# Performance work log

Measured on AMD Instinct MI355X. Metric: run time of the kernel, lower is better.

The kernel has to match this reference:

```python
import jax, jax.numpy as jnp
import numpy as np

LAMBDA_SINK = 0.05  # temperature
NUM_SINK = 10       # Sinkhorn iterations


def setup_inputs() -> dict:
    key = jax.random.key(0)
    log_alpha = jax.random.normal(key, (8, 2048, 2048), dtype=jnp.float32)
    return {"log_alpha": log_alpha}


def reference(log_alpha):
    # gumbel_sinkhorn(log_alpha, temp=lambda_sink, n_iter=num_sink, slack=False)
    la = log_alpha / LAMBDA_SINK

    def body(la, _):
        # row normalization: subtract logsumexp over columns (dim=2)
        la = la - jax.nn.logsumexp(la, axis=2, keepdims=True)
        # column normalization: subtract logsumexp over rows (dim=1)
        la = la - jax.nn.logsumexp(la, axis=1, keepdims=True)
        return la, None

    la, _ = jax.lax.scan(body, la, None, length=NUM_SINK)
    return jnp.exp(la)  # doubly-stochastic (approx) matrix
```

## Files before the change

### kernel.cpp

```cpp
#include <hip/hip_runtime.h>
#include <math.h>

#define NB 8
#define NN 2048
#define SCALE2 28.853900817779268f
#define RPW 8
#define BROWS 32
#define CHB (NN / BROWS)

#if __has_builtin(__builtin_amdgcn_exp2f)
__device__ __forceinline__ float fexp2(float x) { return __builtin_amdgcn_exp2f(x); }
#else
__device__ __forceinline__ float fexp2(float x) { return exp2f(x); }
#endif
#if __has_builtin(__builtin_amdgcn_logf)
__device__ __forceinline__ float flog2(float x) { return __builtin_amdgcn_logf(x); }
#else
__device__ __forceinline__ float flog2(float x) { return log2f(x); }
#endif

__device__ __forceinline__ float wave_max(float x) {
#pragma unroll
    for (int off = 32; off >= 1; off >>= 1)
        x = fmaxf(x, __shfl_xor(x, off, 64));
    return x;
}
__device__ __forceinline__ float wave_sum(float x) {
#pragma unroll
    for (int off = 32; off >= 1; off >>= 1)
        x += __shfl_xor(x, off, 64);
    return x;
}

__global__ __launch_bounds__(256, 2) void fused_iter(const float* __restrict__ A,
                                                     const float* __restrict__ v,
                                                     float* __restrict__ u,
                                                     float* __restrict__ ps) {
    const int wid  = threadIdx.x >> 6;
    const int lane = threadIdx.x & 63;
    const int b    = blockIdx.x >> 6;
    const int blk  = blockIdx.x & 63;
    const int row0 = blk * BROWS + wid * RPW;

    float vv[32];
    {
        const float4* v4 = (const float4*)(v + (size_t)b * NN);
#pragma unroll
        for (int k = 0; k < 8; ++k) {
            float4 t = v4[lane + (k << 6)];
            vv[4 * k + 0] = t.x; vv[4 * k + 1] = t.y;
            vv[4 * k + 2] = t.z; vv[4 * k + 3] = t.w;
        }
    }

    float s[32];
#pragma unroll
    for (int i = 0; i < 32; ++i) s[i] = 0.f;

    float nxt[32];
    {
        const float4* a4 = (const float4*)(A + ((size_t)b * NN + row0) * NN);
#pragma unroll
        for (int k = 0; k < 8; ++k) {
            float4 a = a4[lane + (k << 6)];
            nxt[4 * k + 0] = a.x; nxt[4 * k + 1] = a.y;
            nxt[4 * k + 2] = a.z; nxt[4 * k + 3] = a.w;
        }
    }

#pragma unroll 1
    for (int r = 0; r < RPW; ++r) {
        float e[32];
#pragma unroll
        for (int i = 0; i < 32; ++i) e[i] = fmaf(nxt[i], SCALE2, -vv[i]);

        if (r + 1 < RPW) {
            const float4* a4 =
                (const float4*)(A + ((size_t)b * NN + row0 + r + 1) * NN);
#pragma unroll
            for (int k = 0; k < 8; ++k) {
                float4 a = a4[lane + (k << 6)];
                nxt[4 * k + 0] = a.x; nxt[4 * k + 1] = a.y;
                nxt[4 * k + 2] = a.z; nxt[4 * k + 3] = a.w;
            }
        }

        float t[16];
#pragma unroll
        for (int i = 0; i < 16; ++i) t[i] = fmaxf(e[i], e[i + 16]);
#pragma unroll
        for (int off = 8; off >= 1; off >>= 1)
#pragma unroll
            for (int i = 0; i < off; ++i) t[i] = fmaxf(t[i], t[i + off]);
        float m = wave_max(t[0]);

#pragma unroll
        for (int i = 0; i < 32; ++i) e[i] = fexp2(e[i] - m);

#pragma unroll
        for (int i = 0; i < 16; ++i) t[i] = e[i] + e[i + 16];
#pragma unroll
        for (int off = 8; off >= 1; off >>= 1)
#pragma unroll
            for (int i = 0; i < off; ++i) t[i] += t[i + off];
        float S = wave_sum(t[0]);

        if (lane == 0) u[b * NN + row0 + r] = m + flog2(S);
        float rS = __builtin_amdgcn_rcpf(S);
#pragma unroll
        for (int i = 0; i < 32; ++i) s[i] = fmaf(e[i], rS, s[i]);
    }

    __shared__ float4 sm4[4][512];
#pragma unroll
    for (int k = 0; k < 8; ++k)
        sm4[wid][lane + (k << 6)] =
            make_float4(s[4 * k], s[4 * k + 1], s[4 * k + 2], s[4 * k + 3]);
    __syncthreads();

    float4* pbase = (float4*)(ps + ((size_t)b * CHB + blk) * NN);
#pragma unroll
    for (int gg = 0; gg < 2; ++gg) {
        int g = threadIdx.x + (gg << 8);
        float4 x0 = sm4[0][g], x1 = sm4[1][g], x2 = sm4[2][g], x3 = sm4[3][g];
        float4 o;
        o.x = (x0.x + x1.x) + (x2.x + x3.x);
        o.y = (x0.y + x1.y) + (x2.y + x3.y);
        o.z = (x0.z + x1.z) + (x2.z + x3.z);
        o.w = (x0.w + x1.w) + (x2.w + x3.w);
        pbase[g] = o;
    }
}

__global__ __launch_bounds__(256) void combine(const float* __restrict__ ps,
                                               float* __restrict__ v) {
    const int l  = threadIdx.x & 63;
    const int g  = threadIdx.x >> 6;
    const int b  = blockIdx.x >> 3;
    const int cb = blockIdx.x & 7;
    const float4* pb = (const float4*)(ps + (size_t)b * CHB * NN)
                     + (size_t)(g * 16) * (NN / 4) + (cb << 6) + l;
    float4 a0 = make_float4(0.f, 0.f, 0.f, 0.f);
    float4 a1 = make_float4(0.f, 0.f, 0.f, 0.f);
#pragma unroll
    for (int i = 0; i < 16; i += 2) {
        float4 x = pb[(size_t)i * (NN / 4)];
        float4 y = pb[(size_t)(i + 1) * (NN / 4)];
        a0.x += x.x; a0.y += x.y; a0.z += x.z; a0.w += x.w;
        a1.x += y.x; a1.y += y.y; a1.z += y.z; a1.w += y.w;
    }
    __shared__ float4 red[4][64];
    float4 c;
    c.x = a0.x + a1.x; c.y = a0.y + a1.y;
    c.z = a0.z + a1.z; c.w = a0.w + a1.w;
    red[g][l] = c;
    __syncthreads();
    if (threadIdx.x < 64) {
        float4 r0 = red[0][l], r1 = red[1][l], r2 = red[2][l], r3 = red[3][l];
        float4 t;
        t.x = (r0.x + r1.x) + (r2.x + r3.x);
        t.y = (r0.y + r1.y) + (r2.y + r3.y);
        t.z = (r0.z + r1.z) + (r2.z + r3.z);
        t.w = (r0.w + r1.w) + (r2.w + r3.w);
        float4* vp = (float4*)(v + (size_t)b * NN) + (cb << 6) + l;
        float4 cur = *vp;
        cur.x += flog2(t.x);
        cur.y += flog2(t.y);
        cur.z += flog2(t.z);
        cur.w += flog2(t.w);
        *vp = cur;
    }
}

__global__ __launch_bounds__(256) void row_lse(const float* __restrict__ A,
                                               const float* __restrict__ v,
                                               float* __restrict__ u) {
    const int wid  = threadIdx.x >> 6;
    const int lane = threadIdx.x & 63;
    const int row  = blockIdx.x * 4 + wid;
    const int b    = row >> 11;
    const float4* a4 = (const float4*)(A + (size_t)row * NN);
    const float4* v4 = (const float4*)(v + (size_t)b * NN);
    float x[32];
#pragma unroll
    for (int k = 0; k < 8; ++k) {
        float4 a  = a4[lane + (k << 6)];
        float4 vv = v4[lane + (k << 6)];
        x[4 * k + 0] = fmaf(a.x, SCALE2, -vv.x);
        x[4 * k + 1] = fmaf(a.y, SCALE2, -vv.y);
        x[4 * k + 2] = fmaf(a.z, SCALE2, -vv.z);
        x[4 * k + 3] = fmaf(a.w, SCALE2, -vv.w);
    }
    float m = -INFINITY;
#pragma unroll
    for (int i = 0; i < 32; ++i) m = fmaxf(m, x[i]);
    m = wave_max(m);
    float s = 0.f;
#pragma unroll
    for (int i = 0; i < 32; ++i) s += fexp2(x[i] - m);
    s = wave_sum(s);
    if (lane == 0) u[row] = m + flog2(s);
}

__global__ __launch_bounds__(256) void col_lse(const float* __restrict__ A,
                                               const float* __restrict__ u,
                                               float* __restrict__ v) {
    const int b    = blockIdx.x >> 6;
    const int tile = blockIdx.x & 63;
    const int ci   = threadIdx.x & 31;
    const int rg   = threadIdx.x >> 5;
    const int col  = (tile << 5) + ci;
    const float* Ab = A + (size_t)b * NN * NN;
    const float* ub = u + b * NN;
    float m0 = -INFINITY, s0 = 0.f, m1 = -INFINITY, s1 = 0.f;
    for (int r = rg; r < NN; r += 16) {
        float x0 = fmaf(Ab[(size_t)r * NN + col], SCALE2, -ub[r]);
        float x1 = fmaf(Ab[(size_t)(r + 8) * NN + col], SCALE2, -ub[r + 8]);
        float nm0 = fmaxf(m0, x0);
        s0 = s0 * fexp2(m0 - nm0) + fexp2(x0 - nm0); m0 = nm0;
        float nm1 = fmaxf(m1, x1);
        s1 = s1 * fexp2(m1 - nm1) + fexp2(x1 - nm1); m1 = nm1;
    }
    float m = fmaxf(m0, m1);
    float s = s0 * fexp2(m0 - m) + s1 * fexp2(m1 - m);
    __shared__ float sm[8][33];
    __shared__ float ss[8][33];
    sm[rg][ci] = m; ss[rg][ci] = s;
    __syncthreads();
    if (threadIdx.x < 32) {
        const int c = threadIdx.x;
        float M = sm[0][c], S = ss[0][c];
#pragma unroll
        for (int g = 1; g < 8; ++g) {
            float mg = sm[g][c], sg = ss[g][c];
            float nM = fmaxf(M, mg);
            S = S * fexp2(M - nM) + sg * fexp2(mg - nM);
            M = nM;
        }
        v[b * NN + (tile << 5) + c] = M + flog2(S);
    }
}

__global__ __launch_bounds__(256) void final_exp(const float* __restrict__ A,
                                                 const float* __restrict__ u,
                                                 const float* __restrict__ v,
                                                 float* __restrict__ out) {
    const int i4    = blockIdx.x * 256 + threadIdx.x;
    const int rglob = i4 >> 9;
    const int c4    = i4 & 511;
    const int b     = rglob >> 11;
    const float uu  = u[rglob];
    float4 a  = ((const float4*)A)[i4];
    float4 vv = ((const float4*)(v + (size_t)b * NN))[c4];
    float4 o;
    o.x = fexp2(fmaf(a.x, SCALE2, -uu) - vv.x);
    o.y = fexp2(fmaf(a.y, SCALE2, -uu) - vv.y);
    o.z = fexp2(fmaf(a.z, SCALE2, -uu) - vv.z);
    o.w = fexp2(fmaf(a.w, SCALE2, -uu) - vv.w);
    ((float4*)out)[i4] = o;
}

extern "C" void kernel_launch(void* const* d_in, const int* in_sizes, int n_in,
                              void* d_out, int out_size, void* d_ws, size_t ws_size,
                              hipStream_t stream) {
    const float* A = (const float*)d_in[0];
    float* out = (float*)d_out;
    float* u  = (float*)d_ws;
    float* v  = u + NB * NN;
    float* ps = v + NB * NN;

    const size_t need =
        ((size_t)2 * NB * NN + (size_t)NB * CHB * NN) * sizeof(float);

    hipMemsetAsync(v, 0, NB * NN * sizeof(float), stream);

    if (ws_size >= need) {
        for (int it = 0; it < 10; ++it) {
            fused_iter<<<NB * CHB, 256, 0, stream>>>(A, v, u, ps);
            combine<<<NB * 8, 256, 0, stream>>>(ps, v);
        }
    } else {
        for (int it = 0; it < 10; ++it) {
            row_lse<<<NB * NN / 4, 256, 0, stream>>>(A, v, u);
            col_lse<<<NB * (NN / 32), 256, 0, stream>>>(A, u, v);
        }
    }
    final_exp<<<NB * NN * NN / 1024, 256, 0, stream>>>(A, u, v, out);
}
```

Baseline: 494.0 us.

## Switch Sinkhorn iterations to the linear domain using a precomputed exponentiated matrix

```diff
diff --git a/kernel.cpp b/kernel.cpp
--- a/kernel.cpp
+++ b/kernel.cpp
@@ -4,6 +4,11 @@
 #define NB 8
 #define NN 2048
 #define SCALE2 28.853900817779268f
+
+#define RPWX 4
+#define BROWSX 16
+#define CHBX (NN / BROWSX)
+
 #define RPW 8
 #define BROWS 32
 #define CHB (NN / BROWS)
@@ -32,6 +37,249 @@
     return x;
 }
 
+
+__global__ __launch_bounds__(256, 3) void k0_exp(const float* __restrict__ A,
+                                                 float* __restrict__ X,
+                                                 float* __restrict__ ru,
+                                                 float* __restrict__ ps) {
+    const int wid  = threadIdx.x >> 6;
+    const int lane = threadIdx.x & 63;
+    const int b    = blockIdx.x >> 7;
+    const int blk  = blockIdx.x & 127;
+    const int row0 = blk * BROWSX + wid * RPWX;
+
+    float s[32];
+#pragma unroll
+    for (int i = 0; i < 32; ++i) s[i] = 0.f;
+
+    float nxt[32];
+    {
+        const float4* a4 = (const float4*)(A + ((size_t)b * NN + row0) * NN);
+#pragma unroll
+        for (int k = 0; k < 8; ++k) {
+            float4 a = a4[lane + (k << 6)];
+            nxt[4 * k + 0] = a.x; nxt[4 * k + 1] = a.y;
+            nxt[4 * k + 2] = a.z; nxt[4 * k + 3] = a.w;
+        }
+    }
+
+#pragma unroll 1
+    for (int r = 0; r < RPWX; ++r) {
+        float e[32];
+#pragma unroll
+        for (int i = 0; i < 32; ++i) e[i] = nxt[i] * SCALE2;
+
+        if (r + 1 < RPWX) {
+            const float4* a4 =
+                (const float4*)(A + ((size_t)b * NN + row0 + r + 1) * NN);
+#pragma unroll
+            for (int k = 0; k < 8; ++k) {
+                float4 a = a4[lane + (k << 6)];
+                nxt[4 * k + 0] = a.x; nxt[4 * k + 1] = a.y;
+                nxt[4 * k + 2] = a.z; nxt[4 * k + 3] = a.w;
+            }
+        }
+
+        float t[16];
+#pragma unroll
+        for (int i = 0; i < 16; ++i) t[i] = fmaxf(e[i], e[i + 16]);
+#pragma unroll
+        for (int off = 8; off >= 1; off >>= 1)
+#pragma unroll
+            for (int i = 0; i < off; ++i) t[i] = fmaxf(t[i], t[i + off]);
+        float m = wave_max(t[0]);
+
+#pragma unroll
+        for (int i = 0; i < 32; ++i) e[i] = fexp2(e[i] - m);
+
+        float4* xo = (float4*)(X + ((size_t)b * NN + row0 + r) * NN);
+#pragma unroll
+        for (int k = 0; k < 8; ++k)
+            xo[lane + (k << 6)] =
+                make_float4(e[4 * k], e[4 * k + 1], e[4 * k + 2], e[4 * k + 3]);
+
+#pragma unroll
+        for (int i = 0; i < 16; ++i) t[i] = e[i] + e[i + 16];
+#pragma unroll
+        for (int off = 8; off >= 1; off >>= 1)
+#pragma unroll
+            for (int i = 0; i < off; ++i) t[i] += t[i + off];
+        float S = wave_sum(t[0]);
+        float rS = __builtin_amdgcn_rcpf(S);
+        if (lane == 0) ru[b * NN + row0 + r] = rS;
+#pragma unroll
+        for (int i = 0; i < 32; ++i) s[i] = fmaf(e[i], rS, s[i]);
+    }
+
+    __shared__ float4 sm4[4][512];
+#pragma unroll
+    for (int k = 0; k < 8; ++k)
+        sm4[wid][lane + (k << 6)] =
+            make_float4(s[4 * k], s[4 * k + 1], s[4 * k + 2], s[4 * k + 3]);
+    __syncthreads();
+
+    float4* pbase = (float4*)(ps + ((size_t)b * CHBX + blk) * NN);
+#pragma unroll
+    for (int gg = 0; gg < 2; ++gg) {
+        int g = threadIdx.x + (gg << 8);
+        float4 x0 = sm4[0][g], x1 = sm4[1][g], x2 = sm4[2][g], x3 = sm4[3][g];
+        float4 o;
+        o.x = (x0.x + x1.x) + (x2.x + x3.x);
+        o.y = (x0.y + x1.y) + (x2.y + x3.y);
+        o.z = (x0.z + x1.z) + (x2.z + x3.z);
+        o.w = (x0.w + x1.w) + (x2.w + x3.w);
+        pbase[g] = o;
+    }
+}
+
+__global__ __launch_bounds__(256, 3) void kI_iter(const float* __restrict__ X,
+                                                  const float* __restrict__ w,
+                                                  float* __restrict__ ru,
+                                                  float* __restrict__ ps) {
+    const int wid  = threadIdx.x >> 6;
+    const int lane = threadIdx.x & 63;
+    const int b    = blockIdx.x >> 7;
+    const int blk  = blockIdx.x & 127;
+    const int row0 = blk * BROWSX + wid * RPWX;
+
+    float wv[32];
+    {
+        const float4* w4 = (const float4*)(w + (size_t)b * NN);
+#pragma unroll
+        for (int k = 0; k < 8; ++k) {
+            float4 t = w4[lane + (k << 6)];
+            wv[4 * k + 0] = t.x; wv[4 * k + 1] = t.y;
+            wv[4 * k + 2] = t.z; wv[4 * k + 3] = t.w;
+        }
+    }
+
+    float s[32];
+#pragma unroll
+    for (int i = 0; i < 32; ++i) s[i] = 0.f;
+
+    float nxt[32];
+    {
+        const float4* x4 = (const float4*)(X + ((size_t)b * NN + row0) * NN);
+#pragma unroll
+        for (int k = 0; k < 8; ++k) {
+            float4 a = x4[lane + (k << 6)];
+            nxt[4 * k + 0] = a.x; nxt[4 * k + 1] = a.y;
+            nxt[4 * k + 2] = a.z; nxt[4 * k + 3] = a.w;
+        }
+    }
+
+#pragma unroll 1
+    for (int r = 0; r < RPWX; ++r) {
+        float p[32];
+#pragma unroll
+        for (int i = 0; i < 32; ++i) p[i] = nxt[i] * wv[i];
+
+        if (r + 1 < RPWX) {
+            const float4* x4 =
+                (const float4*)(X + ((size_t)b * NN + row0 + r + 1) * NN);
+#pragma unroll
+            for (int k = 0; k < 8; ++k) {
+                float4 a = x4[lane + (k << 6)];
+                nxt[4 * k + 0] = a.x; nxt[4 * k + 1] = a.y;
+                nxt[4 * k + 2] = a.z; nxt[4 * k + 3] = a.w;
+            }
+        }
+
+        float t[16];
+#pragma unroll
+        for (int i = 0; i < 16; ++i) t[i] = p[i] + p[i + 16];
+#pragma unroll
+        for (int off = 8; off >= 1; off >>= 1)
+#pragma unroll
+            for (int i = 0; i < off; ++i) t[i] += t[i + off];
+        float S = wave_sum(t[0]);
+        float rS = __builtin_amdgcn_rcpf(S);
+        if (lane == 0) ru[b * NN + row0 + r] = rS;
+#pragma unroll
+        for (int i = 0; i < 32; ++i) s[i] = fmaf(p[i], rS, s[i]);
+    }
+
+    __shared__ float4 sm4[4][512];
+#pragma unroll
+    for (int k = 0; k < 8; ++k)
+        sm4[wid][lane + (k << 6)] =
+            make_float4(s[4 * k], s[4 * k + 1], s[4 * k + 2], s[4 * k + 3]);
+    __syncthreads();
+
+    float4* pbase = (float4*)(ps + ((size_t)b * CHBX + blk) * NN);
+#pragma unroll
+    for (int gg = 0; gg < 2; ++gg) {
+        int g = threadIdx.x + (gg << 8);
+        float4 x0 = sm4[0][g], x1 = sm4[1][g], x2 = sm4[2][g], x3 = sm4[3][g];
+        float4 o;
+        o.x = (x0.x + x1.x) + (x2.x + x3.x);
+        o.y = (x0.y + x1.y) + (x2.y + x3.y);
+        o.z = (x0.z + x1.z) + (x2.z + x3.z);
+        o.w = (x0.w + x1.w) + (x2.w + x3.w);
+        pbase[g] = o;
+    }
+}
+
+__global__ __launch_bounds__(256) void combineX(const float* __restrict__ ps,
+                                                float* __restrict__ w, int first) {
+    const int l  = threadIdx.x & 31;
+    const int g  = threadIdx.x >> 5;
+    const int b  = blockIdx.x >> 4;
+    const int cb = blockIdx.x & 15;
+    const float4* pb = (const float4*)(ps + (size_t)b * CHBX * NN)
+                     + (size_t)(g * 16) * (NN / 4) + (cb << 5) + l;
+    float4 a0 = make_float4(0.f, 0.f, 0.f, 0.f);
+    float4 a1 = make_float4(0.f, 0.f, 0.f, 0.f);
+#pragma unroll
+    for (int i = 0; i < 16; i += 2) {
+        float4 x = pb[(size_t)i * (NN / 4)];
+        float4 y = pb[(size_t)(i + 1) * (NN / 4)];
+        a0.x += x.x; a0.y += x.y; a0.z += x.z; a0.w += x.w;
+        a1.x += y.x; a1.y += y.y; a1.z += y.z; a1.w += y.w;
+    }
+    __shared__ float4 red[8][32];
+    float4 c;
+    c.x = a0.x + a1.x; c.y = a0.y + a1.y;
+    c.z = a0.z + a1.z; c.w = a0.w + a1.w;
+    red[g][l] = c;
+    __syncthreads();
+    if (threadIdx.x < 32) {
+        float4 t = red[0][l];
+#pragma unroll
+        for (int gg = 1; gg < 8; ++gg) {
+            float4 rr = red[gg][l];
+            t.x += rr.x; t.y += rr.y; t.z += rr.z; t.w += rr.w;
+        }
+        float4* wp = (float4*)(w + (size_t)b * NN) + (cb << 5) + l;
+        float4 wo = first ? make_float4(1.f, 1.f, 1.f, 1.f) : *wp;
+        float4 o;
+        o.x = wo.x * __builtin_amdgcn_rcpf(t.x);
+        o.y = wo.y * __builtin_amdgcn_rcpf(t.y);
+        o.z = wo.z * __builtin_amdgcn_rcpf(t.z);
+        o.w = wo.w * __builtin_amdgcn_rcpf(t.w);
+        *wp = o;
+    }
+}
+
+__global__ __launch_bounds__(256) void finalX(const float* __restrict__ X,
+                                              const float* __restrict__ ru,
+                                              const float* __restrict__ w,
+                                              float* __restrict__ out) {
+    const int i4 = blockIdx.x * 256 + threadIdx.x;
+    const int r  = i4 >> 9;
+    const int c4 = i4 & 511;
+    const int b  = r >> 11;
+    const float rr = ru[r];
+    float4 x  = ((const float4*)X)[i4];
+    float4 ww = ((const float4*)(w + (size_t)b * NN))[c4];
+    float4 o;
+    o.x = x.x * rr * ww.x;
+    o.y = x.y * rr * ww.y;
+    o.z = x.z * rr * ww.z;
+    o.w = x.w * rr * ww.w;
+    ((float4*)out)[i4] = o;
+}
+
 __global__ __launch_bounds__(256, 2) void fused_iter(const float* __restrict__ A,
                                                      const float* __restrict__ v,
                                                      float* __restrict__ u,
@@ -52,11 +300,9 @@
             vv[4 * k + 2] = t.z; vv[4 * k + 3] = t.w;
         }
     }
-
     float s[32];
 #pragma unroll
     for (int i = 0; i < 32; ++i) s[i] = 0.f;
-
     float nxt[32];
     {
         const float4* a4 = (const float4*)(A + ((size_t)b * NN + row0) * NN);
@@ -67,13 +313,11 @@
             nxt[4 * k + 2] = a.z; nxt[4 * k + 3] = a.w;
         }
     }
-
 #pragma unroll 1
     for (int r = 0; r < RPW; ++r) {
         float e[32];
 #pragma unroll
         for (int i = 0; i < 32; ++i) e[i] = fmaf(nxt[i], SCALE2, -vv[i]);
-
         if (r + 1 < RPW) {
             const float4* a4 =
                 (const float4*)(A + ((size_t)b * NN + row0 + r + 1) * NN);
@@ -84,7 +328,6 @@
                 nxt[4 * k + 2] = a.z; nxt[4 * k + 3] = a.w;
             }
         }
-
         float t[16];
 #pragma unroll
         for (int i = 0; i < 16; ++i) t[i] = fmaxf(e[i], e[i + 16]);
@@ -93,10 +336,8 @@
 #pragma unroll
             for (int i = 0; i < off; ++i) t[i] = fmaxf(t[i], t[i + off]);
         float m = wave_max(t[0]);
-
 #pragma unroll
         for (int i = 0; i < 32; ++i) e[i] = fexp2(e[i] - m);
-
 #pragma unroll
         for (int i = 0; i < 16; ++i) t[i] = e[i] + e[i + 16];
 #pragma unroll
@@ -104,20 +345,17 @@
 #pragma unroll
             for (int i = 0; i < off; ++i) t[i] += t[i + off];
         float S = wave_sum(t[0]);
-
         if (lane == 0) u[b * NN + row0 + r] = m + flog2(S);
         float rS = __builtin_amdgcn_rcpf(S);
 #pragma unroll
         for (int i = 0; i < 32; ++i) s[i] = fmaf(e[i], rS, s[i]);
     }
-
     __shared__ float4 sm4[4][512];
 #pragma unroll
     for (int k = 0; k < 8; ++k)
         sm4[wid][lane + (k << 6)] =
             make_float4(s[4 * k], s[4 * k + 1], s[4 * k + 2], s[4 * k + 3]);
     __syncthreads();
-
     float4* pbase = (float4*)(ps + ((size_t)b * CHB + blk) * NN);
 #pragma unroll
     for (int gg = 0; gg < 2; ++gg) {
@@ -265,25 +503,41 @@
                               hipStream_t stream) {
     const float* A = (const float*)d_in[0];
     float* out = (float*)d_out;
+
+    float* ru   = (float*)d_ws;
+    float* wcol = ru + NB * NN;
+    float* psX  = wcol + NB * NN;
+    float* X    = psX + (size_t)NB * CHBX * NN;
+    const size_t need_x = ((size_t)2 * NB * NN + (size_t)NB * CHBX * NN +
+                           (size_t)NB * NN * NN) * sizeof(float);
+
     float* u  = (float*)d_ws;
     float* v  = u + NB * NN;
     float* ps = v + NB * NN;
-
-    const size_t need =
+    const size_t need_f =
         ((size_t)2 * NB * NN + (size_t)NB * CHB * NN) * sizeof(float);
 
-    hipMemsetAsync(v, 0, NB * NN * sizeof(float), stream);
-
-    if (ws_size >= need) {
+    if (ws_size >= need_x) {
+        k0_exp<<<NB * 128, 256, 0, stream>>>(A, X, ru, psX);
+        combineX<<<NB * 16, 256, 0, stream>>>(psX, wcol, 1);
+        for (int it = 1; it < 10; ++it) {
+            kI_iter<<<NB * 128, 256, 0, stream>>>(X, wcol, ru, psX);
+            combineX<<<NB * 16, 256, 0, stream>>>(psX, wcol, 0);
+        }
+        finalX<<<NB * NN * NN / 1024, 256, 0, stream>>>(X, ru, wcol, out);
+    } else if (ws_size >= need_f) {
+        hipMemsetAsync(v, 0, NB * NN * sizeof(float), stream);
         for (int it = 0; it < 10; ++it) {
             fused_iter<<<NB * CHB, 256, 0, stream>>>(A, v, u, ps);
             combine<<<NB * 8, 256, 0, stream>>>(ps, v);
         }
+        final_exp<<<NB * NN * NN / 1024, 256, 0, stream>>>(A, u, v, out);
     } else {
+        hipMemsetAsync(v, 0, NB * NN * sizeof(float), stream);
         for (int it = 0; it < 10; ++it) {
             row_lse<<<NB * NN / 4, 256, 0, stream>>>(A, v, u);
             col_lse<<<NB * (NN / 32), 256, 0, stream>>>(A, u, v);
         }
-    }
-    final_exp<<<NB * NN * NN / 1024, 256, 0, stream>>>(A, u, v, out);
-}
+        final_exp<<<NB * NN * NN / 1024, 256, 0, stream>>>(A, u, v, out);
+    }
+}
```

Measured after the change: 500.8 us. About the same (+1.4%).
